# Performance work log

Measured on AMD Instinct MI355X. Metric: run time of the kernel, lower is better.

Reference implementation:

```python
import jax, jax.numpy as jnp
import numpy as np

B = 8192
CNN_DIM = 2048
MLP_DIM = 2048
HID = 1024
H = 16
D = HID // H  # 64
EPS = 1e-5


def setup_inputs() -> dict:
    key = jax.random.key(0)
    ks = jax.random.split(key, 12)
    s = 0.02
    return {
        'cnn_out': jax.random.normal(ks[0], (B, CNN_DIM), jnp.float32),
        'mlp_out': jax.random.normal(ks[1], (B, MLP_DIM), jnp.float32),
        # weights stored [in, out] (transposed vs torch nn.Linear)
        'W_cqkv': jax.random.normal(ks[2], (CNN_DIM, 3 * HID), jnp.float32) * s,
        'b_cqkv': jnp.zeros((3 * HID,), jnp.float32),
        'W_mqkv': jax.random.normal(ks[3], (MLP_DIM, 3 * HID), jnp.float32) * s,
        'b_mqkv': jnp.zeros((3 * HID,), jnp.float32),
        'g1': jnp.ones((HID,), jnp.float32),
        'be1': jnp.zeros((HID,), jnp.float32),
        'g2': jnp.ones((HID,), jnp.float32),
        'be2': jnp.zeros((HID,), jnp.float32),
        'W_cproj': jax.random.normal(ks[4], (HID, CNN_DIM), jnp.float32) * s,
        'b_cproj': jnp.zeros((CNN_DIM,), jnp.float32),
        'W_mproj': jax.random.normal(ks[5], (HID, MLP_DIM), jnp.float32) * s,
        'b_mproj': jnp.zeros((MLP_DIM,), jnp.float32),
    }


def _layernorm(x, g, b):
    m = jnp.mean(x, axis=-1, keepdims=True)
    v = jnp.mean((x - m) ** 2, axis=-1, keepdims=True)
    return (x - m) / jnp.sqrt(v + EPS) * g + b


def reference(cnn_out, mlp_out, W_cqkv, b_cqkv, W_mqkv, b_mqkv,
              g1, be1, g2, be2, W_cproj, b_cproj, W_mproj, b_mproj):
    bsz = cnn_out.shape[0]
    scale = 1.0 / jnp.sqrt(jnp.float32(D))

    cqkv = (cnn_out @ W_cqkv + b_cqkv).reshape(bsz, 3, H, D)
    cq, ck, cv = cqkv[:, 0], cqkv[:, 1], cqkv[:, 2]  # each [B,H,D]
    mqkv = (mlp_out @ W_mqkv + b_mqkv).reshape(bsz, 3, H, D)
    mq, mk, mv = mqkv[:, 0], mqkv[:, 1], mqkv[:, 2]

    # branch 1: cnn queries attend over mlp heads -> [B,H,H]
    a1 = jax.nn.softmax(jnp.einsum('bhd,bgd->bhg', cq, mk) * scale, axis=-1)
    ca = jnp.einsum('bhg,bgd->bhd', a1, mv)
    # torch: transpose(1,2).view(B, hidden) -> [B, D, H] flattened
    ca = jnp.swapaxes(ca, 1, 2).reshape(bsz, HID)
    cnn_enh = cnn_out + _layernorm(ca, g1, be1) @ W_cproj + b_cproj

    # branch 2: mlp queries attend over cnn heads
    a2 = jax.nn.softmax(jnp.einsum('bhd,bgd->bhg', mq, ck) * scale, axis=-1)
    ma = jnp.einsum('bhg,bgd->bhd', a2, cv)
    ma = jnp.swapaxes(ma, 1, 2).reshape(bsz, HID)
    mlp_enh = mlp_out + _layernorm(ma, g2, be2) @ W_mproj + b_mproj

    return (cnn_enh, mlp_enh)
```

## Files before the change

kernel.cpp:

```cpp
#include <hip/hip_runtime.h>
#include <hip/hip_bf16.h>
#include <cstdint>
#include <cstddef>

#define NROWS 8192
#define DIM   2048
#define HIDN  1024
#define QKV3  3072
#define EPSV  1e-5f

typedef __attribute__((ext_vector_type(8))) short bf16x8;
typedef __attribute__((ext_vector_type(8))) unsigned short u16x8;
typedef __attribute__((ext_vector_type(4))) float f32x4;

__device__ __forceinline__ unsigned short f2bf(float x) {
    __hip_bfloat16 h = __float2bfloat16(x);
    return *reinterpret_cast<unsigned short*>(&h);
}
__device__ __forceinline__ float bf2f(unsigned short u) {
    return __uint_as_float((unsigned)u << 16);
}

__device__ __forceinline__ void gload_lds16(const void* g, void* l) {
    __builtin_amdgcn_global_load_lds(
        (const __attribute__((address_space(1))) void*)g,
        (__attribute__((address_space(3))) void*)l, 16, 0, 0);
}

template <int N> __device__ __forceinline__ void vmwait() {
    if constexpr (N == 8)      asm volatile("s_waitcnt vmcnt(8)" ::: "memory");
    else if constexpr (N == 4) asm volatile("s_waitcnt vmcnt(4)" ::: "memory");
    else if constexpr (N == 2) asm volatile("s_waitcnt vmcnt(2)" ::: "memory");
    else if constexpr (N == 0) asm volatile("s_waitcnt vmcnt(0)" ::: "memory");
}
__device__ __forceinline__ void barrier_mem() {
    asm volatile("s_barrier" ::: "memory");
}

__global__ __launch_bounds__(256) void prep(
    const float* __restrict__ cnn, unsigned short* __restrict__ Abf_c,
    const float* __restrict__ mlp, unsigned short* __restrict__ Abf_m,
    const float* __restrict__ Wcq, unsigned short* __restrict__ WqT_c,
    const float* __restrict__ Wmq, unsigned short* __restrict__ WqT_m,
    const float* __restrict__ Wcp, unsigned short* __restrict__ WpT_c,
    const float* __restrict__ Wmp, unsigned short* __restrict__ WpT_m) {
    __shared__ float tile[32][33];
    const int bid = blockIdx.x;
    const int t = threadIdx.x;
    if (bid < 16384) {
        const int which = bid >> 13;
        const long b = bid & 8191;
        const float* in = which ? mlp : cnn;
        unsigned short* out = which ? Abf_m : Abf_c;
        const long base = (b * 256 + t) * 8;
        float4 a = *(const float4*)(in + base);
        float4 v = *(const float4*)(in + base + 4);
        uint4 r;
        r.x = (unsigned)f2bf(a.x) | ((unsigned)f2bf(a.y) << 16);
        r.y = (unsigned)f2bf(a.z) | ((unsigned)f2bf(a.w) << 16);
        r.z = (unsigned)f2bf(v.x) | ((unsigned)f2bf(v.y) << 16);
        r.w = (unsigned)f2bf(v.z) | ((unsigned)f2bf(v.w) << 16);
        *(uint4*)(out + base) = r;
        return;
    }
    const int tx = t & 31, ty = t >> 5;
    const float* in;
    unsigned short* out;
    int R, C, l, gw;
    if (bid < 28672) {
        l = bid - 16384;
        const int wq = l / 6144;
        l -= wq * 6144;
        in = wq ? Wmq : Wcq; out = wq ? WqT_m : WqT_c; R = DIM; C = QKV3; gw = 96;
    } else {
        l = bid - 28672;
        const int wp = l / 2048;
        l -= wp * 2048;
        in = wp ? Wmp : Wcp; out = wp ? WpT_m : WpT_c; R = HIDN; C = DIM; gw = 64;
    }
    const int c0 = (l % gw) * 32, r0 = (l / gw) * 32;
#pragma unroll
    for (int i = 0; i < 4; ++i)
        tile[ty + i * 8][tx] = in[(size_t)(r0 + ty + i * 8) * C + c0 + tx];
    __syncthreads();
#pragma unroll
    for (int i = 0; i < 4; ++i)
        out[(size_t)(c0 + ty + i * 8) * R + r0 + tx] = f2bf(tile[tx][ty + i * 8]);
}


__device__ __forceinline__ void stage_half(const unsigned short* __restrict__ G,
                                           int ldK, int rowBase, int kt,
                                           short* ldsHalf, int tid) {
#pragma unroll
    for (int i = 0; i < 2; ++i) {
        const int c = i * 512 + tid;
        const int r = c >> 3;
        const int jl = (c & 7) ^ (r & 7);
        const unsigned short* src = G + (size_t)(rowBase + r) * ldK + kt + jl * 8;
        char* dst = (char*)ldsHalf + (size_t)((i * 512 + (tid & 0x1C0)) * 16);
        gload_lds16(src, dst);
    }
}

__device__ __forceinline__ void load_a4(const short* sAb, int rowA, int o0, int mbase,
                                        bf16x8 (&a)[4][2]) {
#pragma unroll
    for (int m = 0; m < 4; ++m) {
        const char* p = (const char*)sAb + rowA + (mbase + m) * 4096;
        a[m][0] = *(const bf16x8*)(p + o0);
        a[m][1] = *(const bf16x8*)(p + (o0 ^ 64));
    }
}
__device__ __forceinline__ void load_b2(const short* sBb, int rowB, int o0, int nbase,
                                        bf16x8 (&b)[4][2]) {
#pragma unroll
    for (int n = 0; n < 2; ++n) {
        const char* p = (const char*)sBb + rowB + (nbase + n) * 8192;
        b[nbase + n][0] = *(const bf16x8*)(p + o0);
        b[nbase + n][1] = *(const bf16x8*)(p + (o0 ^ 64));
    }
}

#define QUAD(mq, nq)                                                          \
    __builtin_amdgcn_s_setprio(1);                                            \
    _Pragma("unroll") for (int kk_ = 0; kk_ < 2; ++kk_)                       \
    _Pragma("unroll") for (int n_ = 0; n_ < 2; ++n_)                          \
    _Pragma("unroll") for (int m_ = 0; m_ < 4; ++m_)                          \
        acc[(mq) + m_][(nq) + n_] = __builtin_amdgcn_mfma_f32_16x16x32_bf16(  \
            a[m_][kk_], b[(nq) + n_][kk_], acc[(mq) + m_][(nq) + n_], 0, 0, 0); \
    __builtin_amdgcn_s_setprio(0);

#define KTILE(BUF, MODE, KT1, KT2)                                            \
                                                                     \
    load_a4(&sA[BUF][0], rowA, o0, 0, a);                                     \
    if constexpr ((MODE) <= 1)                                                \
        stage_half(Bt, K, tn + 128, (KT1), &sB[(BUF) ^ 1][8192], tid);        \
    if constexpr ((MODE) == 2) { vmwait<2>(); } else { vmwait<8>(); }         \
    barrier_mem();                                                            \
    QUAD(0, 0);                                                               \
                                                                     \
    load_b2(&sB[BUF][0], rowB, o0, 2, b);                                     \
    if constexpr ((MODE) <= 1)                                                \
        stage_half(A, K, tm + 128, (KT1), &sA[(BUF) ^ 1][8192], tid);         \
    if constexpr ((MODE) == 2) { vmwait<0>(); } else { vmwait<8>(); }         \
    barrier_mem();                                                            \
    QUAD(0, 2);                                                               \
                                                                     \
    load_a4(&sA[BUF][0], rowA, o0, 4, a);                                     \
    if constexpr ((MODE) == 0)                                                \
        stage_half(A, K, tm, (KT2), &sA[BUF][0], tid);                        \
    barrier_mem();                                                            \
    QUAD(4, 0);                                                               \
                                                                     \
    if constexpr ((MODE) == 0) {                                              \
        stage_half(Bt, K, tn, (KT2), &sB[BUF][0], tid);                       \
        vmwait<8>();                                                          \
    }                                                                         \
    if constexpr ((MODE) == 1) { vmwait<4>(); }                               \
    barrier_mem();                                                            \
    if constexpr ((MODE) <= 1)                                                \
        load_b2(&sB[(BUF) ^ 1][0], rowB, o0, 0, b);   \
    QUAD(4, 2);

template <int EPI>
__global__ __launch_bounds__(512, 2) void gemm256(
    const unsigned short* __restrict__ A0, const unsigned short* __restrict__ B0t,
    const float* __restrict__ bias0, const float* __restrict__ res0, void* __restrict__ C0,
    const unsigned short* __restrict__ A1, const unsigned short* __restrict__ B1t,
    const float* __restrict__ bias1, const float* __restrict__ res1, void* __restrict__ C1,
    int M, int N, int K, int nbx) {
    __shared__ __align__(16) char smem[131072];
    short (*sA)[16384] = reinterpret_cast<short (*)[16384]>(smem);
    short (*sB)[16384] = reinterpret_cast<short (*)[16384]>(smem + 65536);
    float* smemF = reinterpret_cast<float*>(smem);

    const int tid = threadIdx.x;
    const int nwg = gridDim.x;
    const int ob = blockIdx.x;
    const int swz = (ob & 7) * (nwg >> 3) + (ob >> 3);
    const int per = nbx * (M >> 8);
    const int which = swz >= per ? 1 : 0;
    const int rem = swz - which * per;
    const int by = rem / nbx, bx = rem % nbx;
    const int tm = by << 8, tn = bx << 8;

    const unsigned short* __restrict__ A  = which ? A1 : A0;
    const unsigned short* __restrict__ Bt = which ? B1t : B0t;
    const float* __restrict__ bias  = which ? bias1 : bias0;
    const float* __restrict__ resid = which ? res1 : res0;

    const int w = tid >> 6, l = tid & 63;
    const int wm = w >> 2, wn = w & 3;
    const int lg = l >> 4, lr = l & 15;
    const int o0 = (lg ^ (lr & 7)) << 4;
    const int rowA = (16 * wm + lr) << 7;
    const int rowB = (16 * wn + lr) << 7;

    f32x4 acc[8][4] = {};
    bf16x8 a[4][2], b[4][2];

    const int T = K >> 6;

    stage_half(A,  K, tm,       0,  &sA[0][0],    tid);
    stage_half(Bt, K, tn,       0,  &sB[0][0],    tid);
    stage_half(Bt, K, tn + 128, 0,  &sB[0][8192], tid);
    stage_half(A,  K, tm + 128, 0,  &sA[0][8192], tid);
    stage_half(A,  K, tm,       64, &sA[1][0],    tid);
    stage_half(Bt, K, tn,       64, &sB[1][0],    tid);
    vmwait<8>();
    barrier_mem();
    load_b2(&sB[0][0], rowB, o0, 0, b);

    int kt = 0;
    for (int tt = 0; tt + 4 <= T; tt += 2) {
        KTILE(0, 0, kt + 64, kt + 128);
        KTILE(1, 0, kt + 128, kt + 192);
        kt += 128;
    }
    KTILE(0, 1, kt + 64, 0);
    KTILE(1, 2, 0, 0);

    barrier_mem();
    const int crow_l = 16 * wm + 4 * lg;
    const int ccol_l = 16 * wn + lr;
#pragma unroll
    for (int half = 0; half < 2; ++half) {
#pragma unroll
        for (int mi2 = 0; mi2 < 4; ++mi2) {
            const int lrow = 32 * mi2 + crow_l;
#pragma unroll
            for (int ni = 0; ni < 4; ++ni) {
                const int colg = ccol_l + 64 * ni;
                const float bb = bias[tn + colg];
                const f32x4 v = acc[half * 4 + mi2][ni];
#pragma unroll
                for (int j = 0; j < 4; ++j)
                    smemF[(lrow + j) * 256 + colg] = v[j] + bb;
            }
        }
        barrier_mem();
        const int rowb = tm + half * 128;
        if constexpr (EPI == 0) {
            unsigned short* C = (unsigned short*)(which ? C1 : C0);
#pragma unroll
            for (int i = 0; i < 8; ++i) {
                const int f8 = tid + i * 512;
                const int row = f8 >> 5, c8 = (f8 & 31) * 8;
                const float* p = smemF + f8 * 8;
                u16x8 r;
#pragma unroll
                for (int k = 0; k < 8; ++k) r[k] = f2bf(p[k]);
                *(u16x8*)(C + (size_t)(rowb + row) * N + tn + c8) = r;
            }
        } else {
            float* C = (float*)(which ? C1 : C0);
#pragma unroll
            for (int i = 0; i < 16; ++i) {
                const int f4 = tid + i * 512;
                const int row = f4 >> 6, c4 = (f4 & 63) * 4;
                const size_t idx = (size_t)(rowb + row) * N + tn + c4;
                float4 v = *(const float4*)(smemF + f4 * 4);
                const float4 rr = *(const float4*)(resid + idx);
                v.x += rr.x; v.y += rr.y; v.z += rr.z; v.w += rr.w;
                *(float4*)(C + idx) = v;
            }
        }
        barrier_mem();
    }
}

__device__ __forceinline__ void attn_path(const float* __restrict__ q,
                                          const float* __restrict__ k,
                                          const float* __restrict__ v,
                                          const float* __restrict__ gw,
                                          const float* __restrict__ bw,
                                          unsigned short* __restrict__ out, long b,
                                          float* sS, float* sP, float* red, int t) {
    const int h = t >> 4, gg = t & 15;
    const float* qr = q + h * 68;
    const float* kr = k + gg * 68;
    float s = 0.f;
#pragma unroll
    for (int d = 0; d < 64; d += 4) {
        const float4 qv = *(const float4*)(qr + d);
        const float4 kv = *(const float4*)(kr + d);
        s += qv.x * kv.x + qv.y * kv.y + qv.z * kv.z + qv.w * kv.w;
    }
    sS[h * 17 + gg] = s * 0.125f;
    __syncthreads();
    float mx = -1e30f;
#pragma unroll
    for (int j = 0; j < 16; ++j) mx = fmaxf(mx, sS[h * 17 + j]);
    float sum = 0.f;
#pragma unroll
    for (int j = 0; j < 16; ++j) sum += __expf(sS[h * 17 + j] - mx);
    const float aa = __expf(sS[h * 17 + gg] - mx) / sum;
    sP[h * 17 + gg] = aa;
    __syncthreads();
    float xs[4];
    float lsum = 0.f, lss = 0.f;
#pragma unroll
    for (int r = 0; r < 4; ++r) {
        const int i = t + 256 * r;
        const int d = i >> 4, hh = i & 15;
        float accv = 0.f;
#pragma unroll
        for (int g2 = 0; g2 < 16; ++g2) accv += sP[hh * 17 + g2] * v[g2 * 68 + d];
        xs[r] = accv;
        lsum += accv;
        lss += accv * accv;
    }
#pragma unroll
    for (int off = 32; off > 0; off >>= 1) {
        lsum += __shfl_down(lsum, off);
        lss += __shfl_down(lss, off);
    }
    if ((t & 63) == 0) {
        red[(t >> 6) * 2] = lsum;
        red[(t >> 6) * 2 + 1] = lss;
    }
    __syncthreads();
    const float tot = red[0] + red[2] + red[4] + red[6];
    const float tot2 = red[1] + red[3] + red[5] + red[7];
    const float mean = tot * (1.f / 1024.f);
    const float var = tot2 * (1.f / 1024.f) - mean * mean;
    const float rstd = rsqrtf(var + EPSV);
#pragma unroll
    for (int r = 0; r < 4; ++r) {
        const int i = t + 256 * r;
        const float y = (xs[r] - mean) * rstd * gw[i] + bw[i];
        out[b * 1024 + i] = f2bf(y);
    }
}

__global__ __launch_bounds__(256) void attn_ln(const unsigned short* __restrict__ qkv_c,
                                               const unsigned short* __restrict__ qkv_m,
                                               const float* __restrict__ g1,
                                               const float* __restrict__ be1,
                                               const float* __restrict__ g2,
                                               const float* __restrict__ be2,
                                               unsigned short* __restrict__ ln1,
                                               unsigned short* __restrict__ ln2) {
    __shared__ float qc[48 * 68];
    __shared__ float qm[48 * 68];
    __shared__ float sS[16 * 17];
    __shared__ float sP[16 * 17];
    __shared__ float red[8];
    const int t = threadIdx.x;
    const long b = blockIdx.x;

    const unsigned short* rc = qkv_c + b * QKV3;
    const unsigned short* rm = qkv_m + b * QKV3;
#pragma unroll
    for (int it = 0; it < 3; ++it) {
        const int i0 = t * 4 + it * 1024;
        ushort4 vc = *(const ushort4*)(rc + i0);
        ushort4 vm = *(const ushort4*)(rm + i0);
        const int o = (i0 >> 6) * 68 + (i0 & 63);
        qc[o + 0] = bf2f(vc.x); qc[o + 1] = bf2f(vc.y);
        qc[o + 2] = bf2f(vc.z); qc[o + 3] = bf2f(vc.w);
        qm[o + 0] = bf2f(vm.x); qm[o + 1] = bf2f(vm.y);
        qm[o + 2] = bf2f(vm.z); qm[o + 3] = bf2f(vm.w);
    }
    __syncthreads();
    attn_path(qc, qm + 16 * 68, qm + 32 * 68, g1, be1, ln1, b, sS, sP, red, t);
    __syncthreads();
    attn_path(qm, qc + 16 * 68, qc + 32 * 68, g2, be2, ln2, b, sS, sP, red, t);
}

extern "C" void kernel_launch(void* const* d_in, const int* in_sizes, int n_in,
                              void* d_out, int out_size, void* d_ws, size_t ws_size,
                              hipStream_t stream) {
    const float* cnn    = (const float*)d_in[0];
    const float* mlp    = (const float*)d_in[1];
    const float* W_cqkv = (const float*)d_in[2];
    const float* b_cqkv = (const float*)d_in[3];
    const float* W_mqkv = (const float*)d_in[4];
    const float* b_mqkv = (const float*)d_in[5];
    const float* g1     = (const float*)d_in[6];
    const float* be1    = (const float*)d_in[7];
    const float* g2     = (const float*)d_in[8];
    const float* be2    = (const float*)d_in[9];
    const float* W_cproj = (const float*)d_in[10];
    const float* b_cproj = (const float*)d_in[11];
    const float* W_mproj = (const float*)d_in[12];
    const float* b_mproj = (const float*)d_in[13];
    float* out = (float*)d_out;
    char* ws = (char*)d_ws;

    unsigned short* Abf_c = (unsigned short*)(ws + 0);
    unsigned short* Abf_m = (unsigned short*)(ws + 33554432);
    unsigned short* WqT_c = (unsigned short*)(ws + 67108864);
    unsigned short* WqT_m = (unsigned short*)(ws + 79691776);
    unsigned short* qkv_c = (unsigned short*)(ws + 92274688);
    unsigned short* qkv_m = (unsigned short*)(ws + 142606336);
    unsigned short* ln1   = (unsigned short*)(ws + 0);
    unsigned short* ln2   = (unsigned short*)(ws + 16777216);
    unsigned short* WpT_c = (unsigned short*)(ws + 192937984);
    unsigned short* WpT_m = (unsigned short*)(ws + 197132288);

    prep<<<32768, 256, 0, stream>>>(cnn, Abf_c, mlp, Abf_m,
                                    W_cqkv, WqT_c, W_mqkv, WqT_m,
                                    W_cproj, WpT_c, W_mproj, WpT_m);

    gemm256<0><<<768, 512, 0, stream>>>(Abf_c, WqT_c, b_cqkv, nullptr, qkv_c,
                                        Abf_m, WqT_m, b_mqkv, nullptr, qkv_m,
                                        NROWS, QKV3, DIM, QKV3 / 256);

    attn_ln<<<NROWS, 256, 0, stream>>>(qkv_c, qkv_m, g1, be1, g2, be2, ln1, ln2);

    gemm256<1><<<512, 512, 0, stream>>>(ln1, WpT_c, b_cproj, cnn, out,
                                        ln2, WpT_m, b_mproj, mlp, out + (size_t)NROWS * DIM,
                                        NROWS, DIM, HIDN, DIM / 256);
}
```

Before: 391.0 us.

## Switch GEMM inner loop to 32x32x16 MFMA with reworked fragment loads

Replaces the 16x16x32 bf16 MFMA tiling with 32x32x16 MFMA instructions, so each wave holds 4x2 accumulators of 16 floats and loads A/B fragments in four k-slices per 64-wide tile. This changes the LDS read pattern, the wave-to-tile mapping and the epilogue scatter into shared memory. The aim is fewer LDS reads per FLOP and fewer MFMA issues. The trade-offs are a different LDS bank-conflict profile under the existing XOR swizzle and higher register pressure.

```diff
diff --git a/kernel.cpp b/kernel.cpp
--- a/kernel.cpp
+++ b/kernel.cpp
@@ -12,6 +12,7 @@
 typedef __attribute__((ext_vector_type(8))) short bf16x8;
 typedef __attribute__((ext_vector_type(8))) unsigned short u16x8;
 typedef __attribute__((ext_vector_type(4))) float f32x4;
+typedef __attribute__((ext_vector_type(16))) float f32x16;
 
 __device__ __forceinline__ unsigned short f2bf(float x) {
     __hip_bfloat16 h = __float2bfloat16(x);
@@ -103,55 +104,53 @@
     }
 }
 
-__device__ __forceinline__ void load_a4(const short* sAb, int rowA, int o0, int mbase,
-                                        bf16x8 (&a)[4][2]) {
-#pragma unroll
-    for (int m = 0; m < 4; ++m) {
-        const char* p = (const char*)sAb + rowA + (mbase + m) * 4096;
-        a[m][0] = *(const bf16x8*)(p + o0);
-        a[m][1] = *(const bf16x8*)(p + (o0 ^ 64));
-    }
-}
-__device__ __forceinline__ void load_b2(const short* sBb, int rowB, int o0, int nbase,
-                                        bf16x8 (&b)[4][2]) {
-#pragma unroll
-    for (int n = 0; n < 2; ++n) {
-        const char* p = (const char*)sBb + rowB + (nbase + n) * 8192;
-        b[nbase + n][0] = *(const bf16x8*)(p + o0);
-        b[nbase + n][1] = *(const bf16x8*)(p + (o0 ^ 64));
-    }
-}
-
-#define QUAD(mq, nq)                                                          \
+__device__ __forceinline__ void load_a8(const short* sAb, int rowA, int o0, int mbase,
+                                        bf16x8 (&a)[2][4]) {
+#pragma unroll
+    for (int m = 0; m < 2; ++m) {
+        const char* p = (const char*)sAb + rowA + (mbase + m) * 8192;
+#pragma unroll
+        for (int ks = 0; ks < 4; ++ks)
+            a[m][ks] = *(const bf16x8*)(p + (o0 ^ (ks << 5)));
+    }
+}
+__device__ __forceinline__ void load_b4(const short* sBb, int rowB, int o0, int nt,
+                                        bf16x8 (&bn)[4]) {
+    const char* p = (const char*)sBb + rowB + nt * 4096;
+#pragma unroll
+    for (int ks = 0; ks < 4; ++ks)
+        bn[ks] = *(const bf16x8*)(p + (o0 ^ (ks << 5)));
+}
+
+#define QUAD(mq, nt, BN)                                                      \
     __builtin_amdgcn_s_setprio(1);                                            \
-    _Pragma("unroll") for (int kk_ = 0; kk_ < 2; ++kk_)                       \
-    _Pragma("unroll") for (int n_ = 0; n_ < 2; ++n_)                          \
-    _Pragma("unroll") for (int m_ = 0; m_ < 4; ++m_)                          \
-        acc[(mq) + m_][(nq) + n_] = __builtin_amdgcn_mfma_f32_16x16x32_bf16(  \
-            a[m_][kk_], b[(nq) + n_][kk_], acc[(mq) + m_][(nq) + n_], 0, 0, 0); \
+    _Pragma("unroll") for (int ks_ = 0; ks_ < 4; ++ks_)                       \
+    _Pragma("unroll") for (int m_ = 0; m_ < 2; ++m_)                          \
+        acc[(mq) + m_][nt] = __builtin_amdgcn_mfma_f32_32x32x16_bf16(         \
+            a[m_][ks_], BN[ks_], acc[(mq) + m_][nt], 0, 0, 0);                \
     __builtin_amdgcn_s_setprio(0);
 
 #define KTILE(BUF, MODE, KT1, KT2)                                            \
                                                                      \
-    load_a4(&sA[BUF][0], rowA, o0, 0, a);                                     \
+    load_a8(&sA[BUF][0], rowA, o0, 0, a);                                     \
     if constexpr ((MODE) <= 1)                                                \
         stage_half(Bt, K, tn + 128, (KT1), &sB[(BUF) ^ 1][8192], tid);        \
     if constexpr ((MODE) == 2) { vmwait<2>(); } else { vmwait<8>(); }         \
     barrier_mem();                                                            \
-    QUAD(0, 0);                                                               \
+    QUAD(0, 0, b[0]);                                                         \
                                                                      \
-    load_b2(&sB[BUF][0], rowB, o0, 2, b);                                     \
+    load_b4(&sB[BUF][0], rowB, o0, 1, b[1]);                                  \
     if constexpr ((MODE) <= 1)                                                \
         stage_half(A, K, tm + 128, (KT1), &sA[(BUF) ^ 1][8192], tid);         \
     if constexpr ((MODE) == 2) { vmwait<0>(); } else { vmwait<8>(); }         \
     barrier_mem();                                                            \
-    QUAD(0, 2);                                                               \
+    QUAD(0, 1, b[1]);                                                         \
                                                                      \
-    load_a4(&sA[BUF][0], rowA, o0, 4, a);                                     \
+    load_a8(&sA[BUF][0], rowA, o0, 2, a);                                     \
     if constexpr ((MODE) == 0)                                                \
         stage_half(A, K, tm, (KT2), &sA[BUF][0], tid);                        \
     barrier_mem();                                                            \
-    QUAD(4, 0);                                                               \
+    QUAD(2, 0, b[0]);                                                         \
                                                                      \
     if constexpr ((MODE) == 0) {                                              \
         stage_half(Bt, K, tn, (KT2), &sB[BUF][0], tid);                       \
@@ -160,8 +159,8 @@
     if constexpr ((MODE) == 1) { vmwait<4>(); }                               \
     barrier_mem();                                                            \
     if constexpr ((MODE) <= 1)                                                \
-        load_b2(&sB[(BUF) ^ 1][0], rowB, o0, 0, b);   \
-    QUAD(4, 2);
+        load_b4(&sB[(BUF) ^ 1][0], rowB, o0, 0, b[0]);           \
+    QUAD(2, 1, b[1]);
 
 template <int EPI>
 __global__ __launch_bounds__(512, 2) void gemm256(
@@ -192,13 +191,13 @@
 
     const int w = tid >> 6, l = tid & 63;
     const int wm = w >> 2, wn = w & 3;
-    const int lg = l >> 4, lr = l & 15;
-    const int o0 = (lg ^ (lr & 7)) << 4;
-    const int rowA = (16 * wm + lr) << 7;
-    const int rowB = (16 * wn + lr) << 7;
-
-    f32x4 acc[8][4] = {};
-    bf16x8 a[4][2], b[4][2];
+    const int l31 = l & 31, kh = l >> 5;
+    const int o0 = (kh ^ (l & 7)) << 4;
+    const int rowA = (32 * wm + l31) << 7;
+    const int rowB = (64 * wn + l31) << 7;
+
+    f32x16 acc[4][2] = {};
+    bf16x8 a[2][4], b[2][4];
 
     const int T = K >> 6;
 
@@ -210,7 +209,8 @@
     stage_half(Bt, K, tn,       64, &sB[1][0],    tid);
     vmwait<8>();
     barrier_mem();
-    load_b2(&sB[0][0], rowB, o0, 0, b);
+    load_a8(&sA[0][0], rowA, o0, 0, a);
+    load_b4(&sB[0][0], rowB, o0, 0, b[0]);
 
     int kt = 0;
     for (int tt = 0; tt + 4 <= T; tt += 2) {
@@ -222,21 +222,22 @@
     KTILE(1, 2, 0, 0);
 
     barrier_mem();
-    const int crow_l = 16 * wm + 4 * lg;
-    const int ccol_l = 16 * wn + lr;
+    const int lcolw = 64 * wn + l31;
+    const int rsub = 32 * wm + 4 * kh;
 #pragma unroll
     for (int half = 0; half < 2; ++half) {
 #pragma unroll
-        for (int mi2 = 0; mi2 < 4; ++mi2) {
-            const int lrow = 32 * mi2 + crow_l;
-#pragma unroll
-            for (int ni = 0; ni < 4; ++ni) {
-                const int colg = ccol_l + 64 * ni;
-                const float bb = bias[tn + colg];
-                const f32x4 v = acc[half * 4 + mi2][ni];
-#pragma unroll
-                for (int j = 0; j < 4; ++j)
-                    smemF[(lrow + j) * 256 + colg] = v[j] + bb;
+        for (int m2 = 0; m2 < 2; ++m2) {
+            const int mt = 2 * half + m2;
+            const int lrow0 = 64 * m2 + rsub;
+#pragma unroll
+            for (int nt = 0; nt < 2; ++nt) {
+                const int col = lcolw + 32 * nt;
+                const float bb = bias[tn + col];
+                const f32x16 v = acc[mt][nt];
+#pragma unroll
+                for (int r = 0; r < 16; ++r)
+                    smemF[(lrow0 + (r & 3) + 8 * (r >> 2)) * 256 + col] = v[r] + bb;
             }
         }
         barrier_mem();
```

After: 416.6 us. 6.6% more time.
